# Optimization experiments

Hardware: AMD Instinct MI355X
Metric: run time of the kernel (lower is better)

Reference implementation:

```python
import jax, jax.numpy as jnp
import numpy as np

N_NODES = 50000
NEG_SLOPE = 0.2  # PyG GATConv default leaky-relu slope


def _gat_conv(x, edge_index, W, a_src, a_dst, bias, heads, out_ch, concat, num_nodes):
    # x: [N, F_in]; W: [F_in, heads*out_ch]; a_src/a_dst: [heads, out_ch]; bias: [heads*out_ch] or [out_ch]
    h = (x @ W).reshape(num_nodes, heads, out_ch)            # [N,H,C]
    alpha_src = jnp.einsum('nhc,hc->nh', h, a_src)           # [N,H]
    alpha_dst = jnp.einsum('nhc,hc->nh', h, a_dst)           # [N,H]
    src, dst = edge_index[0], edge_index[1]
    e = jax.nn.leaky_relu(alpha_src[src] + alpha_dst[dst], NEG_SLOPE)  # [E,H]
    # segment softmax over incoming edges per destination (self-loops guarantee non-empty segments)
    m = jax.ops.segment_max(e, dst, num_segments=num_nodes)
    e = jnp.exp(e - m[dst])
    denom = jax.ops.segment_sum(e, dst, num_segments=num_nodes)
    alpha = e / denom[dst]                                    # [E,H]
    msg = h[src] * alpha[:, :, None]                          # [E,H,C]
    out = jax.ops.segment_sum(msg, dst, num_segments=num_nodes)  # [N,H,C]
    if concat:
        out = out.reshape(num_nodes, heads * out_ch)
    else:
        out = out.mean(axis=1)
    return out + bias


def _add_self_loops(edge_index, num_nodes):
    loops = jnp.arange(num_nodes, dtype=edge_index.dtype)
    return jnp.concatenate([edge_index, jnp.stack([loops, loops])], axis=1)


def setup_inputs() -> dict:
    key = jax.random.key(0)
    ks = jax.random.split(key, 16)
    N, F_in, H, C_hid, C_out = N_NODES, 128, 4, 64, 64
    E = 800000
    x = jax.random.normal(ks[0], (N, F_in), dtype=jnp.float32)
    edge_index = jax.random.randint(ks[1], (2, E), 0, N, dtype=jnp.int32)
    s = lambda fan: 1.0 / np.sqrt(fan)
    inp = {
        'x': x, 'edge_index': edge_index,
        'W1': jax.random.normal(ks[2], (F_in, H * C_hid), jnp.float32) * s(F_in),
        'a_src1': jax.random.normal(ks[3], (H, C_hid), jnp.float32) * s(C_hid),
        'a_dst1': jax.random.normal(ks[4], (H, C_hid), jnp.float32) * s(C_hid),
        'b1': jnp.zeros((H * C_hid,), jnp.float32),
        'W2': jax.random.normal(ks[5], (H * C_hid, H * C_hid), jnp.float32) * s(H * C_hid),
        'a_src2': jax.random.normal(ks[6], (H, C_hid), jnp.float32) * s(C_hid),
        'a_dst2': jax.random.normal(ks[7], (H, C_hid), jnp.float32) * s(C_hid),
        'b2': jnp.zeros((H * C_hid,), jnp.float32),
        'W3': jax.random.normal(ks[8], (H * C_hid, C_out), jnp.float32) * s(H * C_hid),
        'a_src3': jax.random.normal(ks[9], (1, C_out), jnp.float32) * s(C_out),
        'a_dst3': jax.random.normal(ks[10], (1, C_out), jnp.float32) * s(C_out),
        'b3': jnp.zeros((C_out,), jnp.float32),
    }
    return inp


def reference(x, edge_index, W1, a_src1, a_dst1, b1, W2, a_src2, a_dst2, b2, W3, a_src3, a_dst3, b3):
    N = x.shape[0]
    ei = _add_self_loops(edge_index, N)
    h = _gat_conv(x, ei, W1, a_src1, a_dst1, b1, heads=4, out_ch=64, concat=True, num_nodes=N)
    h = jax.nn.elu(h)
    h = _gat_conv(h, ei, W2, a_src2, a_dst2, b2, heads=4, out_ch=64, concat=True, num_nodes=N)
    h = jax.nn.elu(h)
    out = _gat_conv(h, ei, W3, a_src3, a_dst3, b3, heads=1, out_ch=64, concat=False, num_nodes=N)
    return out
```

## Files before the change

### kernel.cpp

```cpp
#include <hip/hip_runtime.h>
#include <hip/hip_fp16.h>
#include <cstdint>


typedef _Float16 f16;
typedef _Float16 f16x8 __attribute__((ext_vector_type(8)));
typedef float f32x4 __attribute__((ext_vector_type(4)));

__global__ __launch_bounds__(256) void count_kernel(const int* __restrict__ ei,
                                                    int E, int N,
                                                    int* __restrict__ deg) {
  int g = blockIdx.x * 256 + threadIdx.x;
  if (g >= E + N) return;
  int dst = (g < E) ? ei[E + g] : (g - E);
  atomicAdd(&deg[dst], 1);
}

__global__ __launch_bounds__(256) void deg_block_reduce(const int* __restrict__ deg,
                                                        int* __restrict__ bsum, int N) {
  __shared__ int red[4];
  int b = blockIdx.x;
  int v = 0;
#pragma unroll
  for (int s = 0; s < 4; ++s) {
    int idx = b * 1024 + s * 256 + threadIdx.x;
    if (idx < N) v += deg[idx];
  }
  for (int off = 32; off; off >>= 1) v += __shfl_down(v, off);
  if ((threadIdx.x & 63) == 0) red[threadIdx.x >> 6] = v;
  __syncthreads();
  if (threadIdx.x == 0) bsum[b] = red[0] + red[1] + red[2] + red[3];
}

__global__ __launch_bounds__(1024) void small_scan(const int* __restrict__ bsum,
                                                   int* __restrict__ bpre, int NB) {
  __shared__ int buf[1024];
  int v = (threadIdx.x < NB) ? bsum[threadIdx.x] : 0;
  buf[threadIdx.x] = v;
  __syncthreads();
  for (int off = 1; off < 1024; off <<= 1) {
    int tv = (threadIdx.x >= off) ? buf[threadIdx.x - off] : 0;
    __syncthreads();
    buf[threadIdx.x] += tv;
    __syncthreads();
  }
  if (threadIdx.x < NB) bpre[threadIdx.x] = buf[threadIdx.x] - v;
}

__global__ __launch_bounds__(1024) void scan_final(const int* __restrict__ deg,
                                                   const int* __restrict__ bpre,
                                                   int* __restrict__ row_off,
                                                   int* __restrict__ cursor,
                                                   int N, int total) {
  __shared__ int buf[1024];
  int b = blockIdx.x;
  int i = b * 1024 + threadIdx.x;
  int v = (i < N) ? deg[i] : 0;
  buf[threadIdx.x] = v;
  __syncthreads();
  for (int off = 1; off < 1024; off <<= 1) {
    int tv = (threadIdx.x >= off) ? buf[threadIdx.x - off] : 0;
    __syncthreads();
    buf[threadIdx.x] += tv;
    __syncthreads();
  }
  if (i < N) {
    int ro = bpre[b] + buf[threadIdx.x] - v;
    row_off[i] = ro;
    cursor[i] = ro;
  }
  if (i == 0) row_off[N] = total;
}

__global__ __launch_bounds__(256) void scatter_kernel(const int* __restrict__ ei,
                                                      int E, int N,
                                                      int* __restrict__ cursor,
                                                      int* __restrict__ esrc,
                                                      int* __restrict__ edst) {
  int g = blockIdx.x * 256 + threadIdx.x;
  if (g >= E + N) return;
  int src, dst;
  if (g < E) { src = ei[g]; dst = ei[E + g]; }
  else       { src = g - E; dst = src; }
  int pos = atomicAdd(&cursor[dst], 1);
  esrc[pos] = src;
  edst[pos] = dst;
}

__global__ __launch_bounds__(256) void convert_x(const float* __restrict__ x,
                                                 f16* __restrict__ xh, int n) {
  int i = (blockIdx.x * 256 + threadIdx.x) * 4;
  if (i >= n) return;
  float4 v = *reinterpret_cast<const float4*>(&x[i]);
  f16 o[4] = {(f16)v.x, (f16)v.y, (f16)v.z, (f16)v.w};
  *reinterpret_cast<uint2*>(&xh[i]) = *reinterpret_cast<uint2*>(o);
}

__global__ __launch_bounds__(256) void convert_wt(const float* __restrict__ W,
                                                  f16* __restrict__ Wt,
                                                  int K, int Ncol) {
  int t = blockIdx.x * 256 + threadIdx.x;
  if (t >= K * Ncol) return;
  int n = t % Ncol, k = t / Ncol;
  Wt[(size_t)n * K + k] = (f16)W[t];
}

template <int BN>
__global__ __launch_bounds__(256) void mfma_gemm_alpha(
    const f16* __restrict__ A, const f16* __restrict__ Bt,
    f16* __restrict__ Tout,
    const float* __restrict__ avec_src, const float* __restrict__ avec_dst,
    float* __restrict__ asrc, float* __restrict__ adst,
    int M, int K, int Ncol) {
  constexpr int CF = BN / 16;
  constexpr int HL = BN / 64;
  __shared__ f16 As[128][40];
  __shared__ f16 Bs[BN][40];
  int tid = threadIdx.x;
  int wv = tid >> 6, lane = tid & 63;
  int lrow = lane & 15, lkb = lane >> 4;
  int row0 = blockIdx.x * 128, col0 = blockIdx.y * BN;

  f32x4 acc[2][CF];
#pragma unroll
  for (int rf = 0; rf < 2; ++rf)
#pragma unroll
    for (int cf = 0; cf < CF; ++cf) acc[rf][cf] = (f32x4){0.f, 0.f, 0.f, 0.f};

  for (int kk = 0; kk < K; kk += 32) {
#pragma unroll
    for (int q = 0; q < 2; ++q) {
      int slot = tid + q * 256;
      int r = slot >> 2, ko = (slot & 3) << 3;
      int gr = min(row0 + r, M - 1);
      *reinterpret_cast<f16x8*>(&As[r][ko]) =
          *reinterpret_cast<const f16x8*>(&A[(size_t)gr * K + kk + ko]);
    }
#pragma unroll
    for (int q = 0; q < BN / 64; ++q) {
      int slot = tid + q * 256;
      int c = slot >> 2, ko = (slot & 3) << 3;
      *reinterpret_cast<f16x8*>(&Bs[c][ko]) =
          *reinterpret_cast<const f16x8*>(&Bt[(size_t)(col0 + c) * K + kk + ko]);
    }
    __syncthreads();
    f16x8 af[2], bf[CF];
#pragma unroll
    for (int rf = 0; rf < 2; ++rf)
      af[rf] = *reinterpret_cast<f16x8*>(&As[wv * 32 + rf * 16 + lrow][lkb * 8]);
#pragma unroll
    for (int cf = 0; cf < CF; ++cf)
      bf[cf] = *reinterpret_cast<f16x8*>(&Bs[cf * 16 + lrow][lkb * 8]);
#pragma unroll
    for (int rf = 0; rf < 2; ++rf)
#pragma unroll
      for (int cf = 0; cf < CF; ++cf)
        acc[rf][cf] = __builtin_amdgcn_mfma_f32_16x16x32_f16(af[rf], bf[cf],
                                                             acc[rf][cf], 0, 0, 0);
    __syncthreads();
  }

  int Hh = Ncol >> 6;
  float avs[HL][4], avd[HL][4];
#pragma unroll
  for (int hl = 0; hl < HL; ++hl) {
    int hg = (col0 >> 6) + hl;
#pragma unroll
    for (int q = 0; q < 4; ++q) {
      avs[hl][q] = avec_src[hg * 64 + q * 16 + lrow];
      avd[hl][q] = avec_dst[hg * 64 + q * 16 + lrow];
    }
  }

#pragma unroll
  for (int rf = 0; rf < 2; ++rf) {
#pragma unroll
    for (int hl = 0; hl < HL; ++hl) {
      int hg = (col0 >> 6) + hl;
#pragma unroll
      for (int r = 0; r < 4; ++r) {
        float ps = 0.f, pd = 0.f;
#pragma unroll
        for (int q = 0; q < 4; ++q) {
          float v = acc[rf][hl * 4 + q][r];
          ps = fmaf(v, avs[hl][q], ps);
          pd = fmaf(v, avd[hl][q], pd);
        }
#pragma unroll
        for (int off = 1; off < 16; off <<= 1) {
          ps += __shfl_xor(ps, off);
          pd += __shfl_xor(pd, off);
        }
        int row = row0 + wv * 32 + rf * 16 + lkb * 4 + r;
        if (lrow == 0 && row < M) {
          asrc[row * Hh + hg] = ps;
          adst[row * Hh + hg] = pd;
        }
      }
    }
#pragma unroll
    for (int r = 0; r < 4; ++r) {
      int row = row0 + wv * 32 + rf * 16 + lkb * 4 + r;
      if (row < M) {
#pragma unroll
        for (int cf = 0; cf < CF; ++cf)
          Tout[(size_t)row * Ncol + col0 + cf * 16 + lrow] = (f16)acc[rf][cf][r];
      }
    }
  }
}

__global__ __launch_bounds__(256) void edge_weights_h4(
    const int* __restrict__ esrc, const int* __restrict__ edst,
    const float* __restrict__ asrc, const float* __restrict__ adst,
    float* __restrict__ w, int ET) {
  int t = blockIdx.x * 256 + threadIdx.x;
  if (t >= ET * 4) return;
  int j = t >> 2, h = t & 3;
  float e = asrc[esrc[j] * 4 + h] + adst[edst[j] * 4 + h];
  e = fmaxf(e, 0.2f * e);
  w[t] = __expf(e);
}

__global__ __launch_bounds__(256) void edge_weights_h1(
    const int* __restrict__ esrc, const int* __restrict__ edst,
    const float* __restrict__ asrc, const float* __restrict__ adst,
    float* __restrict__ w, int ET) {
  int j = blockIdx.x * 256 + threadIdx.x;
  if (j >= ET) return;
  float e = asrc[esrc[j]] + adst[edst[j]];
  e = fmaxf(e, 0.2f * e);
  w[j] = __expf(e);
}

template <bool ELU>
__global__ __launch_bounds__(256) void aggregate_h4(
    const f16* __restrict__ T16, const int* __restrict__ row_off,
    const int* __restrict__ esrc, const float* __restrict__ w,
    const float* __restrict__ bias, f16* __restrict__ outF, int N) {
  int wv = threadIdx.x >> 6, lane = threadIdx.x & 63;
  int dst = blockIdx.x * 4 + wv;
  if (dst >= N) return;
  int head = lane >> 4;
  int hsel = lane & 48;
  int r0 = row_off[dst], r1 = row_off[dst + 1];
  const char* tbase = reinterpret_cast<const char*>(T16);
  uint loff = (uint)lane * 8;
  float den = 0.f, ax = 0.f, ay = 0.f, az = 0.f, aw = 0.f;
  for (int base = r0; base < r1; base += 8) {
    int jb = base + (lane & 7);
    int sv = 0;
    float wl = 0.f;
    if (jb < r1) {
      sv = esrc[jb];
      wl = w[(jb << 2) + head];
    }
#pragma unroll
    for (int i = 0; i < 8; ++i) {
      int sj = __shfl(sv, i);
      float wj = __shfl(wl, hsel + i);
      den += wj;
      uint2 raw = *reinterpret_cast<const uint2*>(tbase + (((uint)sj << 9) + loff));
      __half2 p0 = *reinterpret_cast<__half2*>(&raw.x);
      __half2 p1 = *reinterpret_cast<__half2*>(&raw.y);
      float2 f0 = __half22float2(p0);
      float2 f1 = __half22float2(p1);
      ax = fmaf(wj, f0.x, ax);
      ay = fmaf(wj, f0.y, ay);
      az = fmaf(wj, f1.x, az);
      aw = fmaf(wj, f1.y, aw);
    }
  }
  float rd = 1.f / den;
  float4 bv = *reinterpret_cast<const float4*>(&bias[lane << 2]);
  float vx = ax * rd + bv.x, vy = ay * rd + bv.y;
  float vz = az * rd + bv.z, vw = aw * rd + bv.w;
  if (ELU) {
    vx = vx > 0.f ? vx : expm1f(vx);
    vy = vy > 0.f ? vy : expm1f(vy);
    vz = vz > 0.f ? vz : expm1f(vz);
    vw = vw > 0.f ? vw : expm1f(vw);
  }
  f16 o[4] = {(f16)vx, (f16)vy, (f16)vz, (f16)vw};
  *reinterpret_cast<uint2*>(&outF[(size_t)dst * 256 + (lane << 2)]) =
      *reinterpret_cast<uint2*>(o);
}

__global__ __launch_bounds__(256) void aggregate_h1(
    const f16* __restrict__ T16, const int* __restrict__ row_off,
    const int* __restrict__ esrc, const float* __restrict__ w,
    const float* __restrict__ bias, float* __restrict__ out, int N) {
  int wv = threadIdx.x >> 6, lane = threadIdx.x & 63;
  int grp = lane >> 4, l = lane & 15;
  int gsel = lane & 48;
  int dst = blockIdx.x * 16 + wv * 4 + grp;
  if (dst >= N) return;
  int r0 = row_off[dst], r1 = row_off[dst + 1];
  const char* tbase = reinterpret_cast<const char*>(T16);
  uint loff = (uint)l * 8;
  float den = 0.f, ax = 0.f, ay = 0.f, az = 0.f, aw = 0.f;
  for (int base = r0; base < r1; base += 8) {
    int jb = base + (l & 7);
    int sv = 0;
    float wl = 0.f;
    if (jb < r1) {
      sv = esrc[jb];
      wl = w[jb];
    }
#pragma unroll
    for (int i = 0; i < 8; ++i) {
      int sj = __shfl(sv, gsel + i);
      float wj = __shfl(wl, gsel + i);
      den += wj;
      uint2 raw = *reinterpret_cast<const uint2*>(tbase + (((uint)sj << 7) + loff));
      __half2 p0 = *reinterpret_cast<__half2*>(&raw.x);
      __half2 p1 = *reinterpret_cast<__half2*>(&raw.y);
      float2 f0 = __half22float2(p0);
      float2 f1 = __half22float2(p1);
      ax = fmaf(wj, f0.x, ax);
      ay = fmaf(wj, f0.y, ay);
      az = fmaf(wj, f1.x, az);
      aw = fmaf(wj, f1.y, aw);
    }
  }
  float rd = 1.f / den;
  float4 v;
  v.x = ax * rd + bias[l * 4 + 0];
  v.y = ay * rd + bias[l * 4 + 1];
  v.z = az * rd + bias[l * 4 + 2];
  v.w = aw * rd + bias[l * 4 + 3];
  *reinterpret_cast<float4*>(&out[(size_t)dst * 64 + l * 4]) = v;
}

extern "C" void kernel_launch(void* const* d_in, const int* in_sizes, int n_in,
                              void* d_out, int out_size, void* d_ws, size_t ws_size,
                              hipStream_t stream) {
  const float* x   = (const float*)d_in[0];
  const int*   ei  = (const int*)d_in[1];
  const float* W1  = (const float*)d_in[2];
  const float* as1 = (const float*)d_in[3];
  const float* ad1 = (const float*)d_in[4];
  const float* b1  = (const float*)d_in[5];
  const float* W2  = (const float*)d_in[6];
  const float* as2 = (const float*)d_in[7];
  const float* ad2 = (const float*)d_in[8];
  const float* b2  = (const float*)d_in[9];
  const float* W3  = (const float*)d_in[10];
  const float* as3 = (const float*)d_in[11];
  const float* ad3 = (const float*)d_in[12];
  const float* b3  = (const float*)d_in[13];
  float* out = (float*)d_out;

  const int Fin = 128, H = 4, C = 64, HC = H * C;
  const int N = in_sizes[0] / Fin;
  const int E = in_sizes[1] / 2;
  const int ET = E + N;
  const int NB = (N + 1023) / 1024;

  f16* xh    = (f16*)d_ws;
  f16* T16   = xh + (size_t)N * Fin;
  f16* F16   = T16 + (size_t)N * HC;
  f16* T16L3 = F16 + (size_t)N * HC;
  f16* Wt1   = T16L3 + (size_t)N * C;
  f16* Wt2   = Wt1 + HC * Fin;
  f16* Wt3   = Wt2 + HC * HC;
  float* asrc = (float*)(Wt3 + C * HC);
  float* adst = asrc + (size_t)N * H;
  float* wbuf = adst + (size_t)N * H;
  int* deg     = (int*)(wbuf + (size_t)ET * 4);
  int* row_off = deg + N;
  int* cursor  = row_off + (N + 1);
  int* bsum    = cursor + N;
  int* bpre    = bsum + NB;
  int* esrc    = bpre + NB;
  int* edst    = esrc + ET;

  hipMemsetAsync(deg, 0, N * sizeof(int), stream);
  count_kernel<<<(ET + 255) / 256, 256, 0, stream>>>(ei, E, N, deg);
  deg_block_reduce<<<NB, 256, 0, stream>>>(deg, bsum, N);
  small_scan<<<1, 1024, 0, stream>>>(bsum, bpre, NB);
  scan_final<<<NB, 1024, 0, stream>>>(deg, bpre, row_off, cursor, N, ET);
  scatter_kernel<<<(ET + 255) / 256, 256, 0, stream>>>(ei, E, N, cursor, esrc, edst);

  convert_x<<<(N * Fin / 4 + 255) / 256, 256, 0, stream>>>(x, xh, N * Fin);
  convert_wt<<<(Fin * HC + 255) / 256, 256, 0, stream>>>(W1, Wt1, Fin, HC);
  convert_wt<<<(HC * HC + 255) / 256, 256, 0, stream>>>(W2, Wt2, HC, HC);
  convert_wt<<<(HC * C + 255) / 256, 256, 0, stream>>>(W3, Wt3, HC, C);

  int gx = (N + 127) / 128;
  int eb4 = (ET * 4 + 255) / 256, eb1 = (ET + 255) / 256;
  int ab4 = (N + 3) / 4;
  int ab1 = (N + 15) / 16;

  mfma_gemm_alpha<128><<<dim3(gx, 2), 256, 0, stream>>>(
      xh, Wt1, T16, as1, ad1, asrc, adst, N, Fin, HC);
  edge_weights_h4<<<eb4, 256, 0, stream>>>(esrc, edst, asrc, adst, wbuf, ET);
  aggregate_h4<true><<<ab4, 256, 0, stream>>>(T16, row_off, esrc, wbuf, b1, F16, N);

  mfma_gemm_alpha<128><<<dim3(gx, 2), 256, 0, stream>>>(
      F16, Wt2, T16, as2, ad2, asrc, adst, N, HC, HC);
  edge_weights_h4<<<eb4, 256, 0, stream>>>(esrc, edst, asrc, adst, wbuf, ET);
  aggregate_h4<true><<<ab4, 256, 0, stream>>>(T16, row_off, esrc, wbuf, b2, F16, N);

  mfma_gemm_alpha<64><<<dim3(gx, 1), 256, 0, stream>>>(
      F16, Wt3, T16L3, as3, ad3, asrc, adst, N, HC, C);
  edge_weights_h1<<<eb1, 256, 0, stream>>>(esrc, edst, asrc, adst, wbuf, ET);
  aggregate_h1<<<ab1, 256, 0, stream>>>(T16L3, row_off, esrc, wbuf, b3, out, N);
}
```

Before: 337.2 us.

## Fuse edge-weight computation into aggregation and fold x conversion into GEMM

Edge attention weights (leaky-relu plus exp) are now computed inside the aggregation kernels from asrc/adst instead of a separate edge_weights pass that wrote an ET×4 float buffer. This also removes the edst array. The fp32-to-fp16 conversion of x moves into the first GEMM's A-tile load, and the GEMM warp tiling changes to 64x64 per wave for BN=128. The aggregation loop now handles 16 edges per chunk with a variable-count loop. The intent is to cut three kernel launches and the large weight-buffer write and read, at the cost of some redundant exp work and a less regular inner loop.

Result: slower. 354.2 us (+5.0%).

```diff
diff --git a/kernel.cpp b/kernel.cpp
--- a/kernel.cpp
+++ b/kernel.cpp
@@ -75,8 +75,7 @@
 __global__ __launch_bounds__(256) void scatter_kernel(const int* __restrict__ ei,
                                                       int E, int N,
                                                       int* __restrict__ cursor,
-                                                      int* __restrict__ esrc,
-                                                      int* __restrict__ edst) {
+                                                      int* __restrict__ esrc) {
   int g = blockIdx.x * 256 + threadIdx.x;
   if (g >= E + N) return;
   int src, dst;
@@ -84,16 +83,6 @@
   else       { src = g - E; dst = src; }
   int pos = atomicAdd(&cursor[dst], 1);
   esrc[pos] = src;
-  edst[pos] = dst;
-}
-
-__global__ __launch_bounds__(256) void convert_x(const float* __restrict__ x,
-                                                 f16* __restrict__ xh, int n) {
-  int i = (blockIdx.x * 256 + threadIdx.x) * 4;
-  if (i >= n) return;
-  float4 v = *reinterpret_cast<const float4*>(&x[i]);
-  f16 o[4] = {(f16)v.x, (f16)v.y, (f16)v.z, (f16)v.w};
-  *reinterpret_cast<uint2*>(&xh[i]) = *reinterpret_cast<uint2*>(o);
 }
 
 __global__ __launch_bounds__(256) void convert_wt(const float* __restrict__ W,
@@ -105,27 +94,29 @@
   Wt[(size_t)n * K + k] = (f16)W[t];
 }
 
-template <int BN>
+template <int BN, bool ACAST>
 __global__ __launch_bounds__(256) void mfma_gemm_alpha(
-    const f16* __restrict__ A, const f16* __restrict__ Bt,
+    const void* __restrict__ Ap_, const f16* __restrict__ Bt,
     f16* __restrict__ Tout,
     const float* __restrict__ avec_src, const float* __restrict__ avec_dst,
     float* __restrict__ asrc, float* __restrict__ adst,
     int M, int K, int Ncol) {
-  constexpr int CF = BN / 16;
-  constexpr int HL = BN / 64;
+  constexpr int RF = (BN == 128) ? 4 : 2;
   __shared__ f16 As[128][40];
   __shared__ f16 Bs[BN][40];
   int tid = threadIdx.x;
   int wv = tid >> 6, lane = tid & 63;
   int lrow = lane & 15, lkb = lane >> 4;
   int row0 = blockIdx.x * 128, col0 = blockIdx.y * BN;
-
-  f32x4 acc[2][CF];
-#pragma unroll
-  for (int rf = 0; rf < 2; ++rf)
-#pragma unroll
-    for (int cf = 0; cf < CF; ++cf) acc[rf][cf] = (f32x4){0.f, 0.f, 0.f, 0.f};
+  int wro = (BN == 128) ? (wv >> 1) * 64 : wv * 32;
+  int wco = (BN == 128) ? (wv & 1) * 64 : 0;
+  int hg = (col0 + wco) >> 6;
+
+  f32x4 acc[RF][4];
+#pragma unroll
+  for (int rf = 0; rf < RF; ++rf)
+#pragma unroll
+    for (int cf = 0; cf < 4; ++cf) acc[rf][cf] = (f32x4){0.f, 0.f, 0.f, 0.f};
 
   for (int kk = 0; kk < K; kk += 32) {
 #pragma unroll
@@ -133,8 +124,17 @@
       int slot = tid + q * 256;
       int r = slot >> 2, ko = (slot & 3) << 3;
       int gr = min(row0 + r, M - 1);
-      *reinterpret_cast<f16x8*>(&As[r][ko]) =
-          *reinterpret_cast<const f16x8*>(&A[(size_t)gr * K + kk + ko]);
+      if (ACAST) {
+        const float* Af = (const float*)Ap_ + (size_t)gr * K + kk + ko;
+        float4 v0 = *reinterpret_cast<const float4*>(Af);
+        float4 v1 = *reinterpret_cast<const float4*>(Af + 4);
+        f16 o[8] = {(f16)v0.x, (f16)v0.y, (f16)v0.z, (f16)v0.w,
+                    (f16)v1.x, (f16)v1.y, (f16)v1.z, (f16)v1.w};
+        *reinterpret_cast<f16x8*>(&As[r][ko]) = *reinterpret_cast<f16x8*>(o);
+      } else {
+        *reinterpret_cast<f16x8*>(&As[r][ko]) =
+            *reinterpret_cast<const f16x8*>((const f16*)Ap_ + (size_t)gr * K + kk + ko);
+      }
     }
 #pragma unroll
     for (int q = 0; q < BN / 64; ++q) {
@@ -144,121 +144,94 @@
           *reinterpret_cast<const f16x8*>(&Bt[(size_t)(col0 + c) * K + kk + ko]);
     }
     __syncthreads();
-    f16x8 af[2], bf[CF];
-#pragma unroll
-    for (int rf = 0; rf < 2; ++rf)
-      af[rf] = *reinterpret_cast<f16x8*>(&As[wv * 32 + rf * 16 + lrow][lkb * 8]);
-#pragma unroll
-    for (int cf = 0; cf < CF; ++cf)
-      bf[cf] = *reinterpret_cast<f16x8*>(&Bs[cf * 16 + lrow][lkb * 8]);
-#pragma unroll
-    for (int rf = 0; rf < 2; ++rf)
-#pragma unroll
-      for (int cf = 0; cf < CF; ++cf)
+    f16x8 af[RF], bf[4];
+#pragma unroll
+    for (int rf = 0; rf < RF; ++rf)
+      af[rf] = *reinterpret_cast<f16x8*>(&As[wro + rf * 16 + lrow][lkb * 8]);
+#pragma unroll
+    for (int cf = 0; cf < 4; ++cf)
+      bf[cf] = *reinterpret_cast<f16x8*>(&Bs[wco + cf * 16 + lrow][lkb * 8]);
+#pragma unroll
+    for (int rf = 0; rf < RF; ++rf)
+#pragma unroll
+      for (int cf = 0; cf < 4; ++cf)
         acc[rf][cf] = __builtin_amdgcn_mfma_f32_16x16x32_f16(af[rf], bf[cf],
                                                              acc[rf][cf], 0, 0, 0);
     __syncthreads();
   }
 
   int Hh = Ncol >> 6;
-  float avs[HL][4], avd[HL][4];
-#pragma unroll
-  for (int hl = 0; hl < HL; ++hl) {
-    int hg = (col0 >> 6) + hl;
-#pragma unroll
-    for (int q = 0; q < 4; ++q) {
-      avs[hl][q] = avec_src[hg * 64 + q * 16 + lrow];
-      avd[hl][q] = avec_dst[hg * 64 + q * 16 + lrow];
-    }
-  }
-
-#pragma unroll
-  for (int rf = 0; rf < 2; ++rf) {
-#pragma unroll
-    for (int hl = 0; hl < HL; ++hl) {
-      int hg = (col0 >> 6) + hl;
-#pragma unroll
-      for (int r = 0; r < 4; ++r) {
-        float ps = 0.f, pd = 0.f;
-#pragma unroll
-        for (int q = 0; q < 4; ++q) {
-          float v = acc[rf][hl * 4 + q][r];
-          ps = fmaf(v, avs[hl][q], ps);
-          pd = fmaf(v, avd[hl][q], pd);
-        }
-#pragma unroll
-        for (int off = 1; off < 16; off <<= 1) {
-          ps += __shfl_xor(ps, off);
-          pd += __shfl_xor(pd, off);
-        }
-        int row = row0 + wv * 32 + rf * 16 + lkb * 4 + r;
-        if (lrow == 0 && row < M) {
-          asrc[row * Hh + hg] = ps;
-          adst[row * Hh + hg] = pd;
-        }
-      }
-    }
+  float avs[4], avd[4];
+#pragma unroll
+  for (int cf = 0; cf < 4; ++cf) {
+    avs[cf] = avec_src[hg * 64 + cf * 16 + lrow];
+    avd[cf] = avec_dst[hg * 64 + cf * 16 + lrow];
+  }
+
+#pragma unroll
+  for (int rf = 0; rf < RF; ++rf) {
 #pragma unroll
     for (int r = 0; r < 4; ++r) {
-      int row = row0 + wv * 32 + rf * 16 + lkb * 4 + r;
+      float ps = 0.f, pd = 0.f;
+#pragma unroll
+      for (int cf = 0; cf < 4; ++cf) {
+        float v = acc[rf][cf][r];
+        ps = fmaf(v, avs[cf], ps);
+        pd = fmaf(v, avd[cf], pd);
+      }
+#pragma unroll
+      for (int off = 1; off < 16; off <<= 1) {
+        ps += __shfl_xor(ps, off);
+        pd += __shfl_xor(pd, off);
+      }
+      int row = row0 + wro + rf * 16 + lkb * 4 + r;
+      if (lrow == 0 && row < M) {
+        asrc[row * Hh + hg] = ps;
+        adst[row * Hh + hg] = pd;
+      }
+    }
+#pragma unroll
+    for (int r = 0; r < 4; ++r) {
+      int row = row0 + wro + rf * 16 + lkb * 4 + r;
       if (row < M) {
 #pragma unroll
-        for (int cf = 0; cf < CF; ++cf)
-          Tout[(size_t)row * Ncol + col0 + cf * 16 + lrow] = (f16)acc[rf][cf][r];
-      }
-    }
-  }
-}
-
-__global__ __launch_bounds__(256) void edge_weights_h4(
-    const int* __restrict__ esrc, const int* __restrict__ edst,
-    const float* __restrict__ asrc, const float* __restrict__ adst,
-    float* __restrict__ w, int ET) {
-  int t = blockIdx.x * 256 + threadIdx.x;
-  if (t >= ET * 4) return;
-  int j = t >> 2, h = t & 3;
-  float e = asrc[esrc[j] * 4 + h] + adst[edst[j] * 4 + h];
-  e = fmaxf(e, 0.2f * e);
-  w[t] = __expf(e);
-}
-
-__global__ __launch_bounds__(256) void edge_weights_h1(
-    const int* __restrict__ esrc, const int* __restrict__ edst,
-    const float* __restrict__ asrc, const float* __restrict__ adst,
-    float* __restrict__ w, int ET) {
-  int j = blockIdx.x * 256 + threadIdx.x;
-  if (j >= ET) return;
-  float e = asrc[esrc[j]] + adst[edst[j]];
-  e = fmaxf(e, 0.2f * e);
-  w[j] = __expf(e);
+        for (int cf = 0; cf < 4; ++cf)
+          Tout[(size_t)row * Ncol + col0 + wco + cf * 16 + lrow] =
+              (f16)acc[rf][cf][r];
+      }
+    }
+  }
 }
 
 template <bool ELU>
 __global__ __launch_bounds__(256) void aggregate_h4(
     const f16* __restrict__ T16, const int* __restrict__ row_off,
-    const int* __restrict__ esrc, const float* __restrict__ w,
-    const float* __restrict__ bias, f16* __restrict__ outF, int N) {
+    const int* __restrict__ esrc, const float* __restrict__ asrc,
+    const float* __restrict__ adst, const float* __restrict__ bias,
+    f16* __restrict__ outF, int N) {
   int wv = threadIdx.x >> 6, lane = threadIdx.x & 63;
   int dst = blockIdx.x * 4 + wv;
   if (dst >= N) return;
   int head = lane >> 4;
-  int hsel = lane & 48;
+  int we = lane >> 2, wh = lane & 3;
+  int ll = lane & 15;
   int r0 = row_off[dst], r1 = row_off[dst + 1];
+  float adjh = adst[dst * 4 + wh];
   const char* tbase = reinterpret_cast<const char*>(T16);
   uint loff = (uint)lane * 8;
   float den = 0.f, ax = 0.f, ay = 0.f, az = 0.f, aw = 0.f;
-  for (int base = r0; base < r1; base += 8) {
-    int jb = base + (lane & 7);
-    int sv = 0;
-    float wl = 0.f;
-    if (jb < r1) {
-      sv = esrc[jb];
-      wl = w[(jb << 2) + head];
-    }
-#pragma unroll
-    for (int i = 0; i < 8; ++i) {
-      int sj = __shfl(sv, i);
-      float wj = __shfl(wl, hsel + i);
+  for (int base = r0; base < r1; base += 16) {
+    int cnt = min(16, r1 - base);
+    int jb = base + ll;
+    int svl = esrc[jb < r1 ? jb : r1 - 1];
+    int sw = __shfl(svl, we);
+    float e = asrc[sw * 4 + wh] + adjh;
+    e = fmaxf(e, 0.2f * e);
+    float wl = (we < cnt) ? __expf(e) : 0.f;
+#pragma unroll 4
+    for (int i = 0; i < cnt; ++i) {
+      int sj = __shfl(svl, i);
+      float wj = __shfl(wl, (i << 2) + head);
       den += wj;
       uint2 raw = *reinterpret_cast<const uint2*>(tbase + (((uint)sj << 9) + loff));
       __half2 p0 = *reinterpret_cast<__half2*>(&raw.x);
@@ -288,28 +261,29 @@
 
 __global__ __launch_bounds__(256) void aggregate_h1(
     const f16* __restrict__ T16, const int* __restrict__ row_off,
-    const int* __restrict__ esrc, const float* __restrict__ w,
-    const float* __restrict__ bias, float* __restrict__ out, int N) {
+    const int* __restrict__ esrc, const float* __restrict__ asrc,
+    const float* __restrict__ adst, const float* __restrict__ bias,
+    float* __restrict__ out, int N) {
   int wv = threadIdx.x >> 6, lane = threadIdx.x & 63;
   int grp = lane >> 4, l = lane & 15;
   int gsel = lane & 48;
   int dst = blockIdx.x * 16 + wv * 4 + grp;
   if (dst >= N) return;
   int r0 = row_off[dst], r1 = row_off[dst + 1];
+  float adj = adst[dst];
   const char* tbase = reinterpret_cast<const char*>(T16);
   uint loff = (uint)l * 8;
   float den = 0.f, ax = 0.f, ay = 0.f, az = 0.f, aw = 0.f;
-  for (int base = r0; base < r1; base += 8) {
-    int jb = base + (l & 7);
-    int sv = 0;
-    float wl = 0.f;
-    if (jb < r1) {
-      sv = esrc[jb];
-      wl = w[jb];
-    }
-#pragma unroll
-    for (int i = 0; i < 8; ++i) {
-      int sj = __shfl(sv, gsel + i);
+  for (int base = r0; base < r1; base += 16) {
+    int cnt = min(16, r1 - base);
+    int jb = base + l;
+    int svl = esrc[jb < r1 ? jb : r1 - 1];
+    float e = asrc[svl] + adj;
+    e = fmaxf(e, 0.2f * e);
+    float wl = (l < cnt) ? __expf(e) : 0.f;
+#pragma unroll 4
+    for (int i = 0; i < cnt; ++i) {
+      int sj = __shfl(svl, gsel + i);
       float wj = __shfl(wl, gsel + i);
       den += wj;
       uint2 raw = *reinterpret_cast<const uint2*>(tbase + (((uint)sj << 7) + loff));
@@ -357,8 +331,7 @@
   const int ET = E + N;
   const int NB = (N + 1023) / 1024;
 
-  f16* xh    = (f16*)d_ws;
-  f16* T16   = xh + (size_t)N * Fin;
+  f16* T16   = (f16*)d_ws;
   f16* F16   = T16 + (size_t)N * HC;
   f16* T16L3 = F16 + (size_t)N * HC;
   f16* Wt1   = T16L3 + (size_t)N * C;
@@ -366,44 +339,37 @@
   f16* Wt3   = Wt2 + HC * HC;
   float* asrc = (float*)(Wt3 + C * HC);
   float* adst = asrc + (size_t)N * H;
-  float* wbuf = adst + (size_t)N * H;
-  int* deg     = (int*)(wbuf + (size_t)ET * 4);
+  int* deg     = (int*)(adst + (size_t)N * H);
   int* row_off = deg + N;
   int* cursor  = row_off + (N + 1);
   int* bsum    = cursor + N;
   int* bpre    = bsum + NB;
   int* esrc    = bpre + NB;
-  int* edst    = esrc + ET;
 
   hipMemsetAsync(deg, 0, N * sizeof(int), stream);
   count_kernel<<<(ET + 255) / 256, 256, 0, stream>>>(ei, E, N, deg);
   deg_block_reduce<<<NB, 256, 0, stream>>>(deg, bsum, N);
   small_scan<<<1, 1024, 0, stream>>>(bsum, bpre, NB);
   scan_final<<<NB, 1024, 0, stream>>>(deg, bpre, row_off, cursor, N, ET);
-  scatter_kernel<<<(ET + 255) / 256, 256, 0, stream>>>(ei, E, N, cursor, esrc, edst);
-
-  convert_x<<<(N * Fin / 4 + 255) / 256, 256, 0, stream>>>(x, xh, N * Fin);
+  scatter_kernel<<<(ET + 255) / 256, 256, 0, stream>>>(ei, E, N, cursor, esrc);
+
   convert_wt<<<(Fin * HC + 255) / 256, 256, 0, stream>>>(W1, Wt1, Fin, HC);
   convert_wt<<<(HC * HC + 255) / 256, 256, 0, stream>>>(W2, Wt2, HC, HC);
   convert_wt<<<(HC * C + 255) / 256, 256, 0, stream>>>(W3, Wt3, HC, C);
 
   int gx = (N + 127) / 128;
-  int eb4 = (ET * 4 + 255) / 256, eb1 = (ET + 255) / 256;
   int ab4 = (N + 3) / 4;
   int ab1 = (N + 15) / 16;
 
-  mfma_gemm_alpha<128><<<dim3(gx, 2), 256, 0, stream>>>(
-      xh, Wt1, T16, as1, ad1, asrc, adst, N, Fin, HC);
-  edge_weights_h4<<<eb4, 256, 0, stream>>>(esrc, edst, asrc, adst, wbuf, ET);
-  aggregate_h4<true><<<ab4, 256, 0, stream>>>(T16, row_off, esrc, wbuf, b1, F16, N);
-
-  mfma_gemm_alpha<128><<<dim3(gx, 2), 256, 0, stream>>>(
+  mfma_gemm_alpha<128, true><<<dim3(gx, 2), 256, 0, stream>>>(
+      x, Wt1, T16, as1, ad1, asrc, adst, N, Fin, HC);
+  aggregate_h4<true><<<ab4, 256, 0, stream>>>(T16, row_off, esrc, asrc, adst, b1, F16, N);
+
+  mfma_gemm_alpha<128, false><<<dim3(gx, 2), 256, 0, stream>>>(
       F16, Wt2, T16, as2, ad2, asrc, adst, N, HC, HC);
-  edge_weights_h4<<<eb4, 256, 0, stream>>>(esrc, edst, asrc, adst, wbuf, ET);
-  aggregate_h4<true><<<ab4, 256, 0, stream>>>(T16, row_off, esrc, wbuf, b2, F16, N);
-
-  mfma_gemm_alpha<64><<<dim3(gx, 1), 256, 0, stream>>>(
+  aggregate_h4<true><<<ab4, 256, 0, stream>>>(T16, row_off, esrc, asrc, adst, b2, F16, N);
+
+  mfma_gemm_alpha<64, false><<<dim3(gx, 1), 256, 0, stream>>>(
       F16, Wt3, T16L3, as3, ad3, asrc, adst, N, HC, C);
-  edge_weights_h1<<<eb1, 256, 0, stream>>>(esrc, edst, asrc, adst, wbuf, ET);
-  aggregate_h1<<<ab1, 256, 0, stream>>>(T16L3, row_off, esrc, wbuf, b3, out, N);
-}
+  aggregate_h1<<<ab1, 256, 0, stream>>>(T16L3, row_off, esrc, asrc, adst, b3, out, N);
+}
```
